# Kernel tuning notes

Measured on AMD Instinct MI355X. Metric: run time of the kernel, lower is better.

The kernel has to match this reference:

```python
import jax, jax.numpy as jnp
import numpy as np

B, L, G, F = 64, 2048, 512, 3072
N = L + G + F            # nodes per graph
NT = B * N               # total flattened nodes
EG = 16384               # edges per graph (shared topology)
E = B * EG
H, D_IN, NUM_LAYERS = 64, 7, 4
EPS = 1e-5


def setup_inputs() -> dict:
    key = jax.random.key(0)
    ks = jax.random.split(key, 8)
    rng = np.random.default_rng(0)
    x = jax.random.normal(ks[0], (NT, D_IN), jnp.float32)
    # shared topology, replicated per graph with node offsets (PyG batched graph)
    eg = rng.integers(0, N, size=(2, EG))
    offs = (np.arange(B) * N)[None, :, None]
    edge_index = jnp.asarray((eg[:, None, :] + offs).reshape(2, E), dtype=jnp.int32)
    base = np.arange(B)[:, None] * N  # per-graph layout: [loc | gen | line]
    loc_idx = jnp.asarray((base + np.arange(0, L)[None, :]).reshape(-1), jnp.int32)
    prod_idx = jnp.asarray((base + np.arange(L, L + G)[None, :]).reshape(-1), jnp.int32)
    line_idx = jnp.asarray((base + np.arange(L + G, N)[None, :]).reshape(-1), jnp.int32)
    # gen->loc incidence [L, G]: each generator sits at one location
    gm = np.zeros((L, G), np.float32)
    gm[rng.integers(0, L, G), np.arange(G)] = 1.0
    # line->loc signed incidence [L, F]: +1 at from-bus, -1 at to-bus
    lm = np.zeros((L, F), np.float32)
    lm[rng.integers(0, L, F), np.arange(F)] += 1.0
    lm[rng.integers(0, L, F), np.arange(F)] -= 1.0
    s = 1.0 / np.sqrt(H)
    se = 1.0 / np.sqrt(D_IN)
    enc_w = jax.random.uniform(ks[1], (H, D_IN), jnp.float32, -se, se)
    enc_b = jnp.zeros((H,), jnp.float32)
    w_rel = jax.random.uniform(ks[2], (NUM_LAYERS, H, H), jnp.float32, -s, s)
    b_rel = jnp.zeros((NUM_LAYERS, H), jnp.float32)
    w_root = jax.random.uniform(ks[3], (NUM_LAYERS, H, H), jnp.float32, -s, s)
    ln_g = jnp.ones((H,), jnp.float32)
    ln_b = jnp.zeros((H,), jnp.float32)
    prod_w = jax.random.uniform(ks[4], (1, H), jnp.float32, -s, s)
    prod_b = jnp.zeros((1,), jnp.float32)
    flow_w = jax.random.uniform(ks[5], (1, H), jnp.float32, -s, s)
    flow_b = jnp.zeros((1,), jnp.float32)
    return {"x": x, "edge_index": edge_index, "prod_idx": prod_idx,
            "line_idx": line_idx, "loc_idx": loc_idx, "enc_w": enc_w, "enc_b": enc_b,
            "ln_g": ln_g, "ln_b": ln_b, "w_rel": w_rel, "b_rel": b_rel, "w_root": w_root,
            "prod_w": prod_w, "prod_b": prod_b, "flow_w": flow_w, "flow_b": flow_b,
            "gen_mask": jnp.asarray(gm), "line_mask": jnp.asarray(lm)}


def reference(x, edge_index, prod_idx, line_idx, loc_idx, enc_w, enc_b, ln_g, ln_b,
              w_rel, b_rel, w_root, prod_w, prod_b, flow_w, flow_b, gen_mask, line_mask):
    h = jax.nn.relu(x @ enc_w.T + enc_b)                       # [NT, H]
    src, dst = edge_index[0], edge_index[1]
    for i in range(NUM_LAYERS):
        # LayerNorm (shared across layers, as in the torch module)
        mu = jnp.mean(h, axis=-1, keepdims=True)
        var = jnp.mean((h - mu) ** 2, axis=-1, keepdims=True)
        hn = (h - mu) * jax.lax.rsqrt(var + EPS) * ln_g + ln_b
        # GraphConv: W_rel * sum_{j in N(i)} h_j + b_rel + W_root * h_i
        agg = jax.ops.segment_sum(hn[src], dst, num_segments=NT)  # gather + scatter-add
        h = jax.nn.relu(agg @ w_rel[i].T + b_rel[i] + hn @ w_root[i].T)
    p = (h[prod_idx] @ prod_w.T + prod_b).reshape(B, G)
    f = (h[line_idx] @ flow_w.T + flow_b).reshape(B, F)
    demand = x[loc_idx, 0].reshape(B, L)
    md = demand - (p @ gen_mask.T + f @ line_mask.T)           # unmet demand [B, L]
    return (p, f, md)
```

## Files before the change

### kernel.cpp

```cpp
#include <hip/hip_runtime.h>

#define B_ 64
#define L_ 2048
#define G_ 512
#define F_ 3072
#define N_ 5632
#define NT_ 360448
#define EG_ 16384
#define E_ 1048576
#define EPS_ 1e-5f
#define KTOT_ 3584
#define KCH_ 448
#define TCAP_ 384
#define OST_ 72

typedef __attribute__((ext_vector_type(8))) short bf8v;
typedef __attribute__((ext_vector_type(4))) float f4v;

__device__ __forceinline__ unsigned short f2bf(float f){
  unsigned int u=__float_as_uint(f);
  unsigned int r=(u + 0x7fffu + ((u>>16)&1u))>>16;
  return (unsigned short)r;
}
__device__ __forceinline__ float bf2f(unsigned short h){
  return __uint_as_float(((unsigned int)h)<<16);
}

__global__ __launch_bounds__(256) void k_prep(const int* __restrict__ ei,
    unsigned short* __restrict__ wcat,
    const float* __restrict__ wrel, const float* __restrict__ wroot,
    int* __restrict__ offT, int* __restrict__ srcs2,
    const float* __restrict__ x, const int* __restrict__ loci, float* __restrict__ outmd,
    unsigned short* __restrict__ hn, const float* __restrict__ ew, const float* __restrict__ eb,
    const float* __restrict__ lng, const float* __restrict__ lnb){
  int bid=blockIdx.x, tid=threadIdx.x;
  if(bid>=600){
    int lane=tid&63, wid=tid>>6;
    int idx=bid-600;
    int gid=idx/88;
    int nb0=(idx%88)*64 + wid*16;
    int ng=lane>>4;
    int lig=lane&15;
    float w[4][7], bias[4], gam[4], bet[4];
    #pragma unroll
    for(int j=0;j<4;j++){
      int c=lig*4+j;
      #pragma unroll
      for(int k=0;k<7;k++) w[j][k]=ew[c*7+k];
      bias[j]=eb[c]; gam[j]=lng[c]; bet[j]=lnb[c];
    }
    #pragma unroll
    for(int t=0;t<4;t++){
      int n=nb0 + t*4 + ng;
      long xrow=((long)gid*N_+n)*7;
      float xv[7];
      #pragma unroll
      for(int k=0;k<7;k++) xv[k]=x[xrow+k];
      float h[4]; float s1=0.f, s2=0.f;
      #pragma unroll
      for(int j=0;j<4;j++){
        float a=bias[j];
        #pragma unroll
        for(int k=0;k<7;k++) a+=xv[k]*w[j][k];
        a=fmaxf(a,0.f);
        h[j]=a; s1+=a; s2+=a*a;
      }
      #pragma unroll
      for(int o=1;o<16;o<<=1){ s1+=__shfl_xor(s1,o,64); s2+=__shfl_xor(s2,o,64); }
      float mu=s1*(1.f/64.f);
      float var=s2*(1.f/64.f)-mu*mu;
      float inv=rsqrtf(var+EPS_);
      unsigned int p0=(unsigned int)f2bf((h[0]-mu)*inv*gam[0]+bet[0])
                    | ((unsigned int)f2bf((h[1]-mu)*inv*gam[1]+bet[1])<<16);
      unsigned int p1=(unsigned int)f2bf((h[2]-mu)*inv*gam[2]+bet[2])
                    | ((unsigned int)f2bf((h[3]-mu)*inv*gam[3]+bet[3])<<16);
      *(uint2*)(hn + (size_t)n*4096 + gid*64 + lig*4) = (uint2){p0,p1};
    }
    return;
  }
  if(bid>=88){
    int i=(bid-88)*256+tid;
    if(i<B_*L_) outmd[i]=x[(long)loci[i]*7];
    if(i<32768){
      int l=i>>13; int rest=i&8191; int n=rest>>7; int k=rest&127;
      float v=(k<64)? wrel[((long)l*64+n)*64+k] : wroot[((long)l*64+n)*64+(k-64)];
      wcat[i]=f2bf(v);
    }
    return;
  }
  __shared__ int cnt64[64], cur64[64];
  int nb=bid*64;
  if(tid<64) cnt64[tid]=0;
  __syncthreads();
  for(int e=tid;e<EG_;e+=1024){
    int d0=ei[E_+e], d1=ei[E_+e+256], d2=ei[E_+e+512], d3=ei[E_+e+768];
    unsigned t0=(unsigned)(d0-nb), t1=(unsigned)(d1-nb);
    unsigned t2=(unsigned)(d2-nb), t3=(unsigned)(d3-nb);
    if(t0<64u) atomicAdd(&cnt64[t0],1);
    if(t1<64u) atomicAdd(&cnt64[t1],1);
    if(t2<64u) atomicAdd(&cnt64[t2],1);
    if(t3<64u) atomicAdd(&cnt64[t3],1);
  }
  __syncthreads();
  if(tid<64){
    int v=cnt64[tid], s=v;
    #pragma unroll
    for(int o=1;o<64;o<<=1){ int u=__shfl_up(s,o,64); if(tid>=o) s+=u; }
    int ex=s-v;
    offT[bid*65+tid]=ex;
    cur64[tid]=ex;
    if(tid==63) offT[bid*65+64]=s;
  }
  __syncthreads();
  for(int e=tid;e<EG_;e+=1024){
    int s0=ei[e],    s1=ei[e+256],    s2=ei[e+512],    s3=ei[e+768];
    int d0=ei[E_+e], d1=ei[E_+e+256], d2=ei[E_+e+512], d3=ei[E_+e+768];
    unsigned t0=(unsigned)(d0-nb), t1=(unsigned)(d1-nb);
    unsigned t2=(unsigned)(d2-nb), t3=(unsigned)(d3-nb);
    if(t0<64u){ int p=atomicAdd(&cur64[t0],1); if(p<TCAP_) srcs2[bid*TCAP_+p]=s0|(d0<<16); }
    if(t1<64u){ int p=atomicAdd(&cur64[t1],1); if(p<TCAP_) srcs2[bid*TCAP_+p]=s1|(d1<<16); }
    if(t2<64u){ int p=atomicAdd(&cur64[t2],1); if(p<TCAP_) srcs2[bid*TCAP_+p]=s2|(d2<<16); }
    if(t3<64u){ int p=atomicAdd(&cur64[t3],1); if(p<TCAP_) srcs2[bid*TCAP_+p]=s3|(d3<<16); }
  }
}

__device__ __forceinline__ void upadd(float* a, uint4 qa, uint4 qb){
  unsigned int t[8]={qa.x,qa.y,qa.z,qa.w,qb.x,qb.y,qb.z,qb.w};
  #pragma unroll
  for(int j=0;j<8;j++){
    a[2*j]   += __uint_as_float(t[j]<<16);
    a[2*j+1] += __uint_as_float(t[j]&0xffff0000u);
  }
}

__device__ __forceinline__ void stw16(char* base, int r, int chunk, unsigned int p0,
                                      unsigned int p1, unsigned int p2, unsigned int p3){
  int byte = r*128 + chunk*16;
  byte ^= (r&7)<<4;
  *(uint4*)(base + byte) = (uint4){p0,p1,p2,p3};
}
__device__ __forceinline__ bf8v ld16(const char* base, int r, int chunk){
  int byte = r*128 + chunk*16;
  byte ^= (r&7)<<4;
  return *(const bf8v*)(base + byte);
}

__global__ __launch_bounds__(256,6) void k_layer(const unsigned short* __restrict__ hs,
    unsigned short* __restrict__ hd, const int* __restrict__ offT, const int* __restrict__ srcs2,
    const unsigned short* __restrict__ wcat, const float* __restrict__ brel,
    const float* __restrict__ lng, const float* __restrict__ lnb, int do_ln){
  __shared__ uint4 aggl4[1152];
  char* agglc=(char*)aggl4;
  int tid=threadIdx.x;
  int w=tid>>6, lane=tid&63;
  int dst0=blockIdx.x*2;

  {
    int jj=dst0>>6, loc=dst0&63;
    int kb=offT[jj*65+loc];
    int ke=offT[jj*65+loc+2];
    const int* esp=srcs2 + jj*TCAP_;
    int co=tid*16;
    float aA[16], aB[16];
    #pragma unroll
    for(int c=0;c<16;c++){ aA[c]=0.f; aB[c]=0.f; }
    for(int k=kb;k<ke;k+=4){
      int nrem=ke-k;
      int i1=(nrem>1)?k+1:k;
      int i2=(nrem>2)?k+2:k;
      int i3=(nrem>3)?k+3:k;
      int u0=esp[k], u1=esp[i1], u2=esp[i2], u3=esp[i3];
      const unsigned short* r0=hs+(size_t)(u0&0xffff)*4096+co;
      const unsigned short* r1=hs+(size_t)(u1&0xffff)*4096+co;
      const unsigned short* r2=hs+(size_t)(u2&0xffff)*4096+co;
      const unsigned short* r3=hs+(size_t)(u3&0xffff)*4096+co;
      uint4 qa0=*(const uint4*)r0, qb0=*(const uint4*)(r0+8);
      uint4 qa1=*(const uint4*)r1, qb1=*(const uint4*)(r1+8);
      uint4 qa2=*(const uint4*)r2, qb2=*(const uint4*)(r2+8);
      uint4 qa3=*(const uint4*)r3, qb3=*(const uint4*)(r3+8);
      if((u0>>16)==dst0) upadd(aA,qa0,qb0); else upadd(aB,qa0,qb0);
      if(nrem>1){ if((u1>>16)==dst0) upadd(aA,qa1,qb1); else upadd(aB,qa1,qb1); }
      if(nrem>2){ if((u2>>16)==dst0) upadd(aA,qa2,qb2); else upadd(aB,qa2,qb2); }
      if(nrem>3){ if((u3>>16)==dst0) upadd(aA,qa3,qb3); else upadd(aB,qa3,qb3); }
    }
    unsigned int pA[8], pB[8];
    #pragma unroll
    for(int j=0;j<8;j++){
      pA[j]=(unsigned int)f2bf(aA[2*j]) | ((unsigned int)f2bf(aA[2*j+1])<<16);
      pB[j]=(unsigned int)f2bf(aB[2*j]) | ((unsigned int)f2bf(aB[2*j+1])<<16);
    }
    int rl=tid>>2, c2=(tid&3)*2;
    stw16(agglc, rl,    c2,   pA[0],pA[1],pA[2],pA[3]);
    stw16(agglc, rl,    c2+1, pA[4],pA[5],pA[6],pA[7]);
    stw16(agglc, 64+rl, c2,   pB[0],pB[1],pB[2],pB[3]);
    stw16(agglc, 64+rl, c2+1, pB[4],pB[5],pB[6],pB[7]);
  }
  __syncthreads();

  int m=lane&15, quad=lane>>4;
  f4v acc[2][4];
  float bias_nt[4], g_nt[4], b_nt[4];
  #pragma unroll
  for(int nt=0;nt<4;nt++){
    int c=nt*16+m;
    bias_nt[nt]=brel[c];
    g_nt[nt]=lng[c]; b_nt[nt]=lnb[c];
    acc[0][nt]=(f4v){0.f,0.f,0.f,0.f};
    acc[1][nt]=(f4v){0.f,0.f,0.f,0.f};
  }
  #pragma unroll
  for(int mt=0;mt<2;mt++){
    int R=w*32+mt*16+m;
    bf8v af0=ld16(agglc,R,quad);
    bf8v af1=ld16(agglc,R,4+quad);
    int dn=dst0+(R>>6), gg=R&63;
    const unsigned short* hrow=hs+(size_t)dn*4096+gg*64;
    bf8v af2=*(const bf8v*)(hrow+quad*8);
    bf8v af3=*(const bf8v*)(hrow+32+quad*8);
    #pragma unroll
    for(int nt=0;nt<4;nt++){
      const unsigned short* wrow=wcat + (long)(nt*16+m)*128 + quad*8;
      bf8v b0=*(const bf8v*)(wrow);
      bf8v b1=*(const bf8v*)(wrow+32);
      bf8v b2=*(const bf8v*)(wrow+64);
      bf8v b3=*(const bf8v*)(wrow+96);
      acc[mt][nt]=__builtin_amdgcn_mfma_f32_16x16x32_bf16(af0,b0,acc[mt][nt],0,0,0);
      acc[mt][nt]=__builtin_amdgcn_mfma_f32_16x16x32_bf16(af1,b1,acc[mt][nt],0,0,0);
      acc[mt][nt]=__builtin_amdgcn_mfma_f32_16x16x32_bf16(af2,b2,acc[mt][nt],0,0,0);
      acc[mt][nt]=__builtin_amdgcn_mfma_f32_16x16x32_bf16(af3,b3,acc[mt][nt],0,0,0);
    }
  }
  __syncthreads();
  unsigned short* ot=(unsigned short*)agglc;

  #pragma unroll
  for(int mt=0;mt<2;mt++){
    float v[4][4];
    #pragma unroll
    for(int nt=0;nt<4;nt++)
      #pragma unroll
      for(int r=0;r<4;r++)
        v[nt][r]=fmaxf(acc[mt][nt][r]+bias_nt[nt],0.f);
    if(do_ln){
      #pragma unroll
      for(int r=0;r<4;r++){
        float rs=v[0][r]+v[1][r]+v[2][r]+v[3][r];
        float rss=v[0][r]*v[0][r]+v[1][r]*v[1][r]+v[2][r]*v[2][r]+v[3][r]*v[3][r];
        #pragma unroll
        for(int o=1;o<16;o<<=1){ rs+=__shfl_xor(rs,o,64); rss+=__shfl_xor(rss,o,64); }
        float mu=rs*(1.f/64.f);
        float var=rss*(1.f/64.f)-mu*mu;
        float inv=rsqrtf(var+EPS_);
        #pragma unroll
        for(int nt=0;nt<4;nt++) v[nt][r]=(v[nt][r]-mu)*inv*g_nt[nt]+b_nt[nt];
      }
    }
    #pragma unroll
    for(int r=0;r<4;r++){
      int R=w*32+mt*16+quad*4+r;
      #pragma unroll
      for(int nt=0;nt<4;nt++) ot[R*OST_ + nt*16+m]=f2bf(v[nt][r]);
    }
  }
  __syncthreads();

  {
    int row=tid>>1, half=tid&1;
    int dnloc=row>>6, gg=row&63;
    const unsigned short* src=ot + row*OST_ + half*32;
    unsigned short* dstp=hd + (size_t)(dst0+dnloc)*4096 + gg*64 + half*32;
    #pragma unroll
    for(int i=0;i<4;i++)
      *(uint4*)(dstp+i*8) = *(const uint4*)(src+i*8);
  }
}

__global__ __launch_bounds__(256) void k_readout2(const unsigned short* __restrict__ h,
    const int* __restrict__ prodi, const int* __restrict__ linei,
    const float* __restrict__ pw, const float* __restrict__ pb,
    const float* __restrict__ fw, const float* __restrict__ fb,
    float* __restrict__ outp, float* __restrict__ outf,
    unsigned short* __restrict__ pfhi, unsigned short* __restrict__ pflo){
  int i=blockIdx.x*256+threadIdx.x;
  const int MP=B_*G_;
  const int MT=MP+B_*F_;
  if(i>=MT) return;
  bool isp=i<MP;
  int j=isp? i : i-MP;
  unsigned nf=(unsigned)(isp? prodi[j] : linei[j]);
  unsigned gg=nf/(unsigned)N_;
  unsigned node=nf-gg*(unsigned)N_;
  const float* wv=isp? pw:fw;
  float acc=isp? pb[0]:fb[0];
  const uint4* hp=(const uint4*)(h + (size_t)node*4096 + gg*64);
  #pragma unroll
  for(int c=0;c<8;c++){
    uint4 u=hp[c];
    unsigned int uu[4]={u.x,u.y,u.z,u.w};
    #pragma unroll
    for(int q=0;q<4;q++){
      float lo=__uint_as_float(uu[q]<<16);
      float hi=__uint_as_float(uu[q]&0xffff0000u);
      acc += lo*wv[c*8+2*q] + hi*wv[c*8+2*q+1];
    }
  }
  int b,kcol;
  if(isp){ outp[j]=acc; b=j/G_; kcol=j%G_; }
  else   { outf[j]=acc; b=j/F_; kcol=G_+j%F_; }
  unsigned short hi=f2bf(acc);
  pfhi[(long)b*KTOT_+kcol]=hi;
  pflo[(long)b*KTOT_+kcol]=f2bf(acc-bf2f(hi));
}

__global__ __launch_bounds__(256) void k_md_gemm(const float* __restrict__ gm, const float* __restrict__ lm,
    const unsigned short* __restrict__ pfhi, const unsigned short* __restrict__ pflo,
    float* __restrict__ outmd){
  int tid=threadIdx.x;
  int w=tid>>6, lane=tid&63;
  int m=lane&15, quad=lane>>4;
  int lb=blockIdx.x>>3, kc=blockIdx.x&7;
  int l=lb*64 + w*16 + m;
  f4v acc[4];
  #pragma unroll
  for(int nt=0;nt<4;nt++) acc[nt]=(f4v){0.f,0.f,0.f,0.f};
  int kk0=kc*KCH_;
  for(int s=0;s<KCH_/32;s++){
    int kk=kk0+s*32;
    const float* ap = (kk<G_)? gm + (long)l*G_ + kk : lm + (long)l*F_ + (kk-G_);
    float4 a0=*(const float4*)(ap+quad*8);
    float4 a1=*(const float4*)(ap+quad*8+4);
    bf8v af;
    af[0]=(short)f2bf(a0.x); af[1]=(short)f2bf(a0.y);
    af[2]=(short)f2bf(a0.z); af[3]=(short)f2bf(a0.w);
    af[4]=(short)f2bf(a1.x); af[5]=(short)f2bf(a1.y);
    af[6]=(short)f2bf(a1.z); af[7]=(short)f2bf(a1.w);
    #pragma unroll
    for(int nt=0;nt<4;nt++){
      int b=nt*16+m;
      const unsigned short* bp=pfhi + (long)b*KTOT_ + kk + quad*8;
      const unsigned short* lp=pflo + (long)b*KTOT_ + kk + quad*8;
      bf8v bh=*(const bf8v*)bp;
      bf8v bl=*(const bf8v*)lp;
      acc[nt]=__builtin_amdgcn_mfma_f32_16x16x32_bf16(af,bh,acc[nt],0,0,0);
      acc[nt]=__builtin_amdgcn_mfma_f32_16x16x32_bf16(af,bl,acc[nt],0,0,0);
    }
  }
  int lrow=lb*64 + w*16 + quad*4;
  #pragma unroll
  for(int r=0;r<4;r++)
    #pragma unroll
    for(int nt=0;nt<4;nt++)
      atomicAdd(&outmd[(long)(nt*16+m)*L_ + lrow+r], -acc[nt][r]);
}

extern "C" void kernel_launch(void* const* d_in, const int* in_sizes, int n_in,
                              void* d_out, int out_size, void* d_ws, size_t ws_size,
                              hipStream_t stream){
  const float* x    =(const float*)d_in[0];
  const int*   ei   =(const int*)d_in[1];
  const int*   prodi=(const int*)d_in[2];
  const int*   linei=(const int*)d_in[3];
  const int*   loci =(const int*)d_in[4];
  const float* ew   =(const float*)d_in[5];
  const float* eb   =(const float*)d_in[6];
  const float* lng  =(const float*)d_in[7];
  const float* lnb  =(const float*)d_in[8];
  const float* wrel =(const float*)d_in[9];
  const float* brel =(const float*)d_in[10];
  const float* wroot=(const float*)d_in[11];
  const float* pw   =(const float*)d_in[12];
  const float* pb   =(const float*)d_in[13];
  const float* fw   =(const float*)d_in[14];
  const float* fb   =(const float*)d_in[15];
  const float* gm   =(const float*)d_in[16];
  const float* lm   =(const float*)d_in[17];

  char* ws=(char*)d_ws;
  unsigned short* hnA =(unsigned short*)ws;
  unsigned short* hnB =hnA + (size_t)NT_*64;
  unsigned short* wcat=hnB + (size_t)NT_*64;
  unsigned short* pfhi=wcat + 32768;
  unsigned short* pflo=pfhi + (size_t)B_*KTOT_;
  int* offT =(int*)(pflo + (size_t)B_*KTOT_);
  int* srcs2=offT + 88*65;

  float* outp =(float*)d_out;
  float* outf =outp + (size_t)B_*G_;
  float* outmd=outf + (size_t)B_*F_;

  k_prep<<<600+NT_/64,256,0,stream>>>(ei,wcat,wrel,wroot,offT,srcs2,
                                      x,loci,outmd,hnA,ew,eb,lng,lnb);
  for(int i=0;i<4;i++){
    const unsigned short* hs=(i&1)?hnB:hnA;
    unsigned short* hd=(i&1)?hnA:hnB;
    k_layer<<<N_/2,256,0,stream>>>(hs,hd,offT,srcs2,wcat+(size_t)i*8192,
        brel+(size_t)i*64,lng,lnb,(i<3)?1:0);
  }
  {
    int MT=B_*(G_+F_);
    k_readout2<<<(MT+255)/256,256,0,stream>>>(hnA,prodi,linei,pw,pb,fw,fb,outp,outf,pfhi,pflo);
  }
  k_md_gemm<<<256,256,0,stream>>>(gm,lm,pfhi,pflo,outmd);
}
```

Measured before the change: 427.2 us.

## Pad per-pair edge lists with zero-row sentinels and write layer outputs directly

```diff
diff --git a/kernel.cpp b/kernel.cpp
--- a/kernel.cpp
+++ b/kernel.cpp
@@ -12,7 +12,7 @@
 #define KTOT_ 3584
 #define KCH_ 448
 #define TCAP_ 384
-#define OST_ 72
+#define HROW_ 5633
 
 typedef __attribute__((ext_vector_type(8))) short bf8v;
 typedef __attribute__((ext_vector_type(4))) float f4v;
@@ -31,7 +31,8 @@
     const float* __restrict__ wrel, const float* __restrict__ wroot,
     int* __restrict__ offT, int* __restrict__ srcs2,
     const float* __restrict__ x, const int* __restrict__ loci, float* __restrict__ outmd,
-    unsigned short* __restrict__ hn, const float* __restrict__ ew, const float* __restrict__ eb,
+    unsigned short* __restrict__ hn, unsigned short* __restrict__ hnb,
+    const float* __restrict__ ew, const float* __restrict__ eb,
     const float* __restrict__ lng, const float* __restrict__ lnb){
   int bid=blockIdx.x, tid=threadIdx.x;
   if(bid>=600){
@@ -85,6 +86,10 @@
       int l=i>>13; int rest=i&8191; int n=rest>>7; int k=rest&127;
       float v=(k<64)? wrel[((long)l*64+n)*64+k] : wroot[((long)l*64+n)*64+(k-64)];
       wcat[i]=f2bf(v);
+    }
+    if(i<4096){
+      hn [(size_t)N_*4096+i]=0;
+      hnb[(size_t)N_*4096+i]=0;
     }
     return;
   }
@@ -103,13 +108,27 @@
   }
   __syncthreads();
   if(tid<64){
-    int v=cnt64[tid], s=v;
+    int v=cnt64[tid];
+    int vo=__shfl_xor(v,1,64);
+    int c0=(tid&1)? vo : v;
+    int psum=v+vo;
+    int ppad=(psum+3)&~3;
+    int wv=(tid&1)? 0 : ppad;
+    int s=wv;
     #pragma unroll
     for(int o=1;o<64;o<<=1){ int u=__shfl_up(s,o,64); if(tid>=o) s+=u; }
-    int ex=s-v;
-    offT[bid*65+tid]=ex;
-    cur64[tid]=ex;
+    int pairstart=s-ppad;
+    int nst=pairstart + ((tid&1)? c0 : 0);
+    offT[bid*65+tid]=nst;
+    cur64[tid]=nst;
     if(tid==63) offT[bid*65+64]=s;
+    if(!(tid&1)){
+      int dw=N_ | ((nb+tid)<<16);
+      for(int q=psum;q<ppad;q++){
+        int p=pairstart+q;
+        if(p<TCAP_) srcs2[bid*TCAP_+p]=dw;
+      }
+    }
   }
   __syncthreads();
   for(int e=tid;e<EG_;e+=1024){
@@ -149,7 +168,7 @@
     unsigned short* __restrict__ hd, const int* __restrict__ offT, const int* __restrict__ srcs2,
     const unsigned short* __restrict__ wcat, const float* __restrict__ brel,
     const float* __restrict__ lng, const float* __restrict__ lnb, int do_ln){
-  __shared__ uint4 aggl4[1152];
+  __shared__ uint4 aggl4[1024];
   char* agglc=(char*)aggl4;
   int tid=threadIdx.x;
   int w=tid>>6, lane=tid&63;
@@ -165,11 +184,7 @@
     #pragma unroll
     for(int c=0;c<16;c++){ aA[c]=0.f; aB[c]=0.f; }
     for(int k=kb;k<ke;k+=4){
-      int nrem=ke-k;
-      int i1=(nrem>1)?k+1:k;
-      int i2=(nrem>2)?k+2:k;
-      int i3=(nrem>3)?k+3:k;
-      int u0=esp[k], u1=esp[i1], u2=esp[i2], u3=esp[i3];
+      int u0=esp[k], u1=esp[k+1], u2=esp[k+2], u3=esp[k+3];
       const unsigned short* r0=hs+(size_t)(u0&0xffff)*4096+co;
       const unsigned short* r1=hs+(size_t)(u1&0xffff)*4096+co;
       const unsigned short* r2=hs+(size_t)(u2&0xffff)*4096+co;
@@ -179,9 +194,9 @@
       uint4 qa2=*(const uint4*)r2, qb2=*(const uint4*)(r2+8);
       uint4 qa3=*(const uint4*)r3, qb3=*(const uint4*)(r3+8);
       if((u0>>16)==dst0) upadd(aA,qa0,qb0); else upadd(aB,qa0,qb0);
-      if(nrem>1){ if((u1>>16)==dst0) upadd(aA,qa1,qb1); else upadd(aB,qa1,qb1); }
-      if(nrem>2){ if((u2>>16)==dst0) upadd(aA,qa2,qb2); else upadd(aB,qa2,qb2); }
-      if(nrem>3){ if((u3>>16)==dst0) upadd(aA,qa3,qb3); else upadd(aB,qa3,qb3); }
+      if((u1>>16)==dst0) upadd(aA,qa1,qb1); else upadd(aB,qa1,qb1);
+      if((u2>>16)==dst0) upadd(aA,qa2,qb2); else upadd(aB,qa2,qb2);
+      if((u3>>16)==dst0) upadd(aA,qa3,qb3); else upadd(aB,qa3,qb3);
     }
     unsigned int pA[8], pB[8];
     #pragma unroll
@@ -230,9 +245,6 @@
       acc[mt][nt]=__builtin_amdgcn_mfma_f32_16x16x32_bf16(af3,b3,acc[mt][nt],0,0,0);
     }
   }
-  __syncthreads();
-  unsigned short* ot=(unsigned short*)agglc;
-
   #pragma unroll
   for(int mt=0;mt<2;mt++){
     float v[4][4];
@@ -258,20 +270,11 @@
     #pragma unroll
     for(int r=0;r<4;r++){
       int R=w*32+mt*16+quad*4+r;
-      #pragma unroll
-      for(int nt=0;nt<4;nt++) ot[R*OST_ + nt*16+m]=f2bf(v[nt][r]);
-    }
-  }
-  __syncthreads();
-
-  {
-    int row=tid>>1, half=tid&1;
-    int dnloc=row>>6, gg=row&63;
-    const unsigned short* src=ot + row*OST_ + half*32;
-    unsigned short* dstp=hd + (size_t)(dst0+dnloc)*4096 + gg*64 + half*32;
-    #pragma unroll
-    for(int i=0;i<4;i++)
-      *(uint4*)(dstp+i*8) = *(const uint4*)(src+i*8);
+      int dn=dst0+(R>>6), gg=R&63;
+      unsigned short* out=hd + (size_t)dn*4096 + gg*64;
+      #pragma unroll
+      for(int nt=0;nt<4;nt++) out[nt*16+m]=f2bf(v[nt][r]);
+    }
   }
 }
 
@@ -377,8 +380,8 @@
 
   char* ws=(char*)d_ws;
   unsigned short* hnA =(unsigned short*)ws;
-  unsigned short* hnB =hnA + (size_t)NT_*64;
-  unsigned short* wcat=hnB + (size_t)NT_*64;
+  unsigned short* hnB =hnA + (size_t)HROW_*4096;
+  unsigned short* wcat=hnB + (size_t)HROW_*4096;
   unsigned short* pfhi=wcat + 32768;
   unsigned short* pflo=pfhi + (size_t)B_*KTOT_;
   int* offT =(int*)(pflo + (size_t)B_*KTOT_);
@@ -389,7 +392,7 @@
   float* outmd=outf + (size_t)B_*F_;
 
   k_prep<<<600+NT_/64,256,0,stream>>>(ei,wcat,wrel,wroot,offT,srcs2,
-                                      x,loci,outmd,hnA,ew,eb,lng,lnb);
+                                      x,loci,outmd,hnA,hnB,ew,eb,lng,lnb);
   for(int i=0;i<4;i++){
     const unsigned short* hs=(i&1)?hnB:hnA;
     unsigned short* hd=(i&1)?hnA:hnB;
```

Result: no change. 432.9 us (+1.3%).

## Write layer outputs directly to global, shrink gather unroll, relax occupancy

Applied to the files above, without the earlier changes.

```diff
diff --git a/kernel.cpp b/kernel.cpp
--- a/kernel.cpp
+++ b/kernel.cpp
@@ -12,7 +12,6 @@
 #define KTOT_ 3584
 #define KCH_ 448
 #define TCAP_ 384
-#define OST_ 72
 
 typedef __attribute__((ext_vector_type(8))) short bf8v;
 typedef __attribute__((ext_vector_type(4))) float f4v;
@@ -145,11 +144,11 @@
   return *(const bf8v*)(base + byte);
 }
 
-__global__ __launch_bounds__(256,6) void k_layer(const unsigned short* __restrict__ hs,
+__global__ __launch_bounds__(256,4) void k_layer(const unsigned short* __restrict__ hs,
     unsigned short* __restrict__ hd, const int* __restrict__ offT, const int* __restrict__ srcs2,
     const unsigned short* __restrict__ wcat, const float* __restrict__ brel,
     const float* __restrict__ lng, const float* __restrict__ lnb, int do_ln){
-  __shared__ uint4 aggl4[1152];
+  __shared__ uint4 aggl4[1024];
   char* agglc=(char*)aggl4;
   int tid=threadIdx.x;
   int w=tid>>6, lane=tid&63;
@@ -164,24 +163,21 @@
     float aA[16], aB[16];
     #pragma unroll
     for(int c=0;c<16;c++){ aA[c]=0.f; aB[c]=0.f; }
-    for(int k=kb;k<ke;k+=4){
-      int nrem=ke-k;
-      int i1=(nrem>1)?k+1:k;
-      int i2=(nrem>2)?k+2:k;
-      int i3=(nrem>3)?k+3:k;
-      int u0=esp[k], u1=esp[i1], u2=esp[i2], u3=esp[i3];
+    int k=kb;
+    for(; k+1<ke; k+=2){
+      int u0=esp[k], u1=esp[k+1];
       const unsigned short* r0=hs+(size_t)(u0&0xffff)*4096+co;
       const unsigned short* r1=hs+(size_t)(u1&0xffff)*4096+co;
-      const unsigned short* r2=hs+(size_t)(u2&0xffff)*4096+co;
-      const unsigned short* r3=hs+(size_t)(u3&0xffff)*4096+co;
       uint4 qa0=*(const uint4*)r0, qb0=*(const uint4*)(r0+8);
       uint4 qa1=*(const uint4*)r1, qb1=*(const uint4*)(r1+8);
-      uint4 qa2=*(const uint4*)r2, qb2=*(const uint4*)(r2+8);
-      uint4 qa3=*(const uint4*)r3, qb3=*(const uint4*)(r3+8);
       if((u0>>16)==dst0) upadd(aA,qa0,qb0); else upadd(aB,qa0,qb0);
-      if(nrem>1){ if((u1>>16)==dst0) upadd(aA,qa1,qb1); else upadd(aB,qa1,qb1); }
-      if(nrem>2){ if((u2>>16)==dst0) upadd(aA,qa2,qb2); else upadd(aB,qa2,qb2); }
-      if(nrem>3){ if((u3>>16)==dst0) upadd(aA,qa3,qb3); else upadd(aB,qa3,qb3); }
+      if((u1>>16)==dst0) upadd(aA,qa1,qb1); else upadd(aB,qa1,qb1);
+    }
+    if(k<ke){
+      int u0=esp[k];
+      const unsigned short* r0=hs+(size_t)(u0&0xffff)*4096+co;
+      uint4 qa0=*(const uint4*)r0, qb0=*(const uint4*)(r0+8);
+      if((u0>>16)==dst0) upadd(aA,qa0,qb0); else upadd(aB,qa0,qb0);
     }
     unsigned int pA[8], pB[8];
     #pragma unroll
@@ -230,9 +226,6 @@
       acc[mt][nt]=__builtin_amdgcn_mfma_f32_16x16x32_bf16(af3,b3,acc[mt][nt],0,0,0);
     }
   }
-  __syncthreads();
-  unsigned short* ot=(unsigned short*)agglc;
-
   #pragma unroll
   for(int mt=0;mt<2;mt++){
     float v[4][4];
@@ -258,20 +251,11 @@
     #pragma unroll
     for(int r=0;r<4;r++){
       int R=w*32+mt*16+quad*4+r;
-      #pragma unroll
-      for(int nt=0;nt<4;nt++) ot[R*OST_ + nt*16+m]=f2bf(v[nt][r]);
-    }
-  }
-  __syncthreads();
-
-  {
-    int row=tid>>1, half=tid&1;
-    int dnloc=row>>6, gg=row&63;
-    const unsigned short* src=ot + row*OST_ + half*32;
-    unsigned short* dstp=hd + (size_t)(dst0+dnloc)*4096 + gg*64 + half*32;
-    #pragma unroll
-    for(int i=0;i<4;i++)
-      *(uint4*)(dstp+i*8) = *(const uint4*)(src+i*8);
+      int dn=dst0+(R>>6), gg=R&63;
+      unsigned short* out=hd + (size_t)dn*4096 + gg*64;
+      #pragma unroll
+      for(int nt=0;nt<4;nt++) out[nt*16+m]=f2bf(v[nt][r]);
+    }
   }
 }
 
```

Result: faster. 380.0 us (-11.0%).
